# Performance work log

Hardware: AMD Instinct MI355X
Metric: run time of the kernel (lower is better)

## Reference

```python
import jax, jax.numpy as jnp
import numpy as np
from jax import lax

B, N, C_IN = 8, 16384, 32
NPOINT = 1024
RADII = (0.5, 1.0)
NSAMPLES = (16, 32)
MLPS = ((35, 32, 64), (35, 64, 128))  # first dim includes +3 for use_xyz


def setup_inputs():
    key = jax.random.key(0)
    ks = jax.random.split(key, 20)
    inp = {
        'xyz': jax.random.normal(ks[0], (B, N, 3), jnp.float32),
        'features': jax.random.normal(ks[1], (B, C_IN, N), jnp.float32),
    }
    i = 2
    for bi, spec in enumerate(MLPS):
        for li in range(len(spec) - 1):
            cin, cout = spec[li], spec[li + 1]
            inp['w%d_%d' % (bi, li)] = jax.random.normal(ks[i], (cout, cin), jnp.float32) * np.float32(1.0 / np.sqrt(cin)); i += 1
            inp['s%d_%d' % (bi, li)] = jax.random.uniform(ks[i], (cout,), jnp.float32, minval=0.5, maxval=1.5); i += 1
            inp['b%d_%d' % (bi, li)] = jax.random.normal(ks[i], (cout,), jnp.float32) * 0.1; i += 1
    return inp


def _fps(xyz, npoint):
    # iterative D-FPS, start from index 0 (matches CUDA furthest_point_sampling)
    Bb, Nn, _ = xyz.shape
    def body(carry, _):
        dists, far = carry
        centroid = jnp.take_along_axis(xyz, far[:, None, None], axis=1)  # (B,1,3)
        d = jnp.sum((xyz - centroid) ** 2, axis=-1)                       # (B,N)
        dists = jnp.minimum(dists, d)
        return (dists, jnp.argmax(dists, axis=-1).astype(jnp.int32)), far
    init = (jnp.full((Bb, Nn), 1e10, jnp.float32), jnp.zeros((Bb,), jnp.int32))
    _, idx = lax.scan(body, init, None, length=npoint)
    return idx.T  # (B, npoint)


def _ball_query(dist2, radius, nsample):
    # first-nsample-in-index-order semantics of pointnet2 ball_query;
    # empty slots padded with first hit (0 if no hit at all)
    Nn = dist2.shape[-1]
    scores = jnp.where(dist2 < radius * radius, jnp.arange(Nn, dtype=jnp.int32), Nn)
    neg, _ = lax.top_k(-scores, nsample)  # nsample smallest indices
    idx = -neg
    first = jnp.where(idx[..., :1] == Nn, 0, idx[..., :1])
    return jnp.where(idx == Nn, first, idx)


def _forward(xyz, features, params):
    fwx = jnp.concatenate([xyz.transpose(0, 2, 1), features], axis=1)   # (B,3+C,N)
    fps_idx = _fps(xyz, NPOINT)                                          # (B,P) int32
    new_xyz = jnp.take_along_axis(xyz, fps_idx[:, :, None], axis=1)      # (B,P,3)
    # pairwise squared distances via gemm (B,P,N)
    xx = jnp.sum(xyz * xyz, axis=-1)
    qq = jnp.sum(new_xyz * new_xyz, axis=-1)
    dist2 = qq[:, :, None] + xx[:, None, :] - 2.0 * jnp.einsum('bpd,bnd->bpn', new_xyz, xyz)
    centers = new_xyz.transpose(0, 2, 1)[..., None]                      # (B,3,P,1)
    outs = []
    for k in range(len(RADII)):
        idx = _ball_query(dist2, RADII[k], NSAMPLES[k])                  # (B,P,S)
        grouped = jax.vmap(lambda f, i: f[:, i])(fwx, idx)               # (B,3+C,P,S)
        x = jnp.concatenate([grouped[:, :3] - centers, grouped[:, 3:]], axis=1)
        for (w, s, b) in params[k]:
            # 1x1 Conv2d (no bias) + eval-mode BN folded into (s,b) + ReLU
            x = jax.nn.relu(jnp.einsum('oc,bcps->bops', w, x) * s[None, :, None, None] + b[None, :, None, None])
        outs.append(jnp.max(x, axis=-1))                                 # max_pool over nsample
    return new_xyz, jnp.concatenate(outs, axis=1)                        # (B,P,3), (B,192,P)


def reference(xyz, features, w0_0, s0_0, b0_0, w0_1, s0_1, b0_1, w1_0, s1_0, b1_0, w1_1, s1_1, b1_1):
    params = [[(w0_0, s0_0, b0_0), (w0_1, s0_1, b0_1)],
              [(w1_0, s1_0, b1_0), (w1_1, s1_1, b1_1)]]
    return _forward(xyz, features, params)
```

## Files before the change

### kernel.cpp

```cpp
#include <hip/hip_runtime.h>

#define B 8
#define N 16384
#define C_IN 32
#define P 1024

typedef float v2f __attribute__((ext_vector_type(2)));
typedef unsigned long long ull;

#define R8(OP) OP(0) OP(1) OP(2) OP(3) OP(4) OP(5) OP(6) OP(7)

__device__ __forceinline__ v2f pk_add(v2f a, v2f b) {
  v2f d; asm("v_pk_add_f32 %0, %1, %2" : "=v"(d) : "v"(a), "v"(b)); return d;
}
__device__ __forceinline__ v2f pk_mul(v2f a, v2f b) {
  v2f d; asm("v_pk_mul_f32 %0, %1, %2" : "=v"(d) : "v"(a), "v"(b)); return d;
}
__device__ __forceinline__ float negf(float x) {
  return __int_as_float(__float_as_int(x) ^ 0x80000000);
}

template <int CTRL>
__device__ __forceinline__ float dpp_fmax(float v) {
  float o = __int_as_float(__builtin_amdgcn_update_dpp(
      __float_as_int(v), __float_as_int(v), CTRL, 0xF, 0xF, false));
  return fmaxf(v, o);
}

__global__ __launch_bounds__(1024)
void fps_kernel(const float* __restrict__ xyz, float* __restrict__ new_xyz)
{
  __shared__ __align__(16) float sx[N];
  __shared__ __align__(16) float sy[N];
  __shared__ ull slot[2];

  const int b = blockIdx.x;
  const int t = threadIdx.x;
  const float* xb = xyz + (size_t)b * (N * 3);

  if (t == 0) { slot[0] = ~0ull; slot[1] = ~0ull; }

#define FPS_DECL(j) v2f pzp##j, dmp##j; dmp##j.x = 1e10f; dmp##j.y = 1e10f;
  R8(FPS_DECL)
#define FPS_LOADP(j) {                                                         \
    const int n0 = (t << 2) + ((j >> 1) << 12) + ((j & 1) << 1);               \
    const float2 ld0 = *(const float2*)&xb[(size_t)n0 * 3 + 0];     \
    const float2 ld1 = *(const float2*)&xb[(size_t)n0 * 3 + 2];     \
    const float2 ld2 = *(const float2*)&xb[(size_t)n0 * 3 + 4];     \
    sx[n0]     = ld0.x;  sy[n0]     = ld0.y;                                   \
    sx[n0 + 1] = ld1.y;  sy[n0 + 1] = ld2.x;                                   \
    pzp##j.x   = ld1.x;  pzp##j.y   = ld2.y;                                   \
    asm volatile("" : "+v"(pzp##j)); }
  R8(FPS_LOADP)

  float cz = xb[2];
  __syncthreads();
  float cx = sx[0], cy = sy[0];
  int sel = 0, msel = 0;

  for (int iter = 0; iter < P; ++iter) {
    msel = (t == iter) ? sel : msel;
    if (iter == P - 1) break;

    v2f cxx, cyy, czz;
    { float v = negf(cx); cxx.x = v; cxx.y = v; }
    { float v = negf(cy); cyy.x = v; cyy.y = v; }
    { float v = negf(cz); czz.x = v; czz.y = v; }

    v2f sq0, sq1, sq2, sq3, sq4, sq5, sq6, sq7;
#define FPS_XY(i, ja, jb) {                                                    \
      const int n0 = (t << 2) + ((i) << 12);                                   \
      v2f xl = *(const v2f*)&sx[n0];  v2f xh = *(const v2f*)&sx[n0 + 2];       \
      v2f yl = *(const v2f*)&sy[n0];  v2f yh = *(const v2f*)&sy[n0 + 2];       \
      v2f dxl = pk_add(xl, cxx), dyl = pk_add(yl, cyy);                        \
      v2f dxh = pk_add(xh, cxx), dyh = pk_add(yh, cyy);                        \
      sq##ja = pk_add(pk_mul(dxl, dxl), pk_mul(dyl, dyl));                     \
      sq##jb = pk_add(pk_mul(dxh, dxh), pk_mul(dyh, dyh)); }
    FPS_XY(0, 0, 1)
    FPS_XY(1, 2, 3)
    FPS_XY(2, 4, 5)
    FPS_XY(3, 6, 7)

    float bestv = -1.0f;
    int   s = 0;
#define FPS_Z(j) {                                                             \
      v2f dz = pk_add(pzp##j, czz);                                            \
      v2f dd = pk_add(sq##j, pk_mul(dz, dz));                                  \
      dmp##j.x = fminf(dmp##j.x, dd.x);                                        \
      dmp##j.y = fminf(dmp##j.y, dd.y);                                        \
      bool b0 = dmp##j.x > bestv;                                              \
      bestv = b0 ? dmp##j.x : bestv;  s = b0 ? (2 * (j))     : s;              \
      bool b1 = dmp##j.y > bestv;                                              \
      bestv = b1 ? dmp##j.y : bestv;  s = b1 ? (2 * (j) + 1) : s; }
    R8(FPS_Z)

    float wm = bestv;
    wm = dpp_fmax<0xB1>(wm);
    wm = dpp_fmax<0x4E>(wm);
    wm = dpp_fmax<0x141>(wm);
    wm = dpp_fmax<0x140>(wm);
    wm = dpp_fmax<0x142>(wm);
    wm = dpp_fmax<0x143>(wm);
    const float wmax = __int_as_float(
        __builtin_amdgcn_readlane(__float_as_int(wm), 63));

    if (bestv == wmax) {
      int nn = (t << 2) + ((s & 12) << 10) + (s & 3);
      unsigned inv = ~__float_as_uint(bestv);
      ull key = ((ull)(unsigned)(P - 1 - iter) << 46) |
                ((ull)inv << 14) | (ull)(unsigned)nn;
      atomicMin(&slot[iter & 1], key);
    }
    __syncthreads();

    ull k = slot[iter & 1];
    sel = __builtin_amdgcn_readfirstlane((int)((unsigned)k & 0x3FFFu));
    cx = sx[sel];
    cy = sy[sel];
    cz = xb[(size_t)sel * 3 + 2];
  }

  {
    const int n = msel;
    size_t o = ((size_t)b * P + t) * 3;
    new_xyz[o + 0] = sx[n];
    new_xyz[o + 1] = sy[n];
    new_xyz[o + 2] = xb[(size_t)n * 3 + 2];
  }
#undef FPS_DECL
#undef FPS_LOADP
#undef FPS_XY
#undef FPS_Z
}

__global__ __launch_bounds__(256) void ballq_kernel(
    const float* __restrict__ xyz, const float* __restrict__ new_xyz,
    int* __restrict__ idx0, int* __restrict__ idx1)
{
  const int wid  = blockIdx.x * 4 + (threadIdx.x >> 6);
  const int lane = threadIdx.x & 63;
  const int b = wid >> 10;
  const int p = wid & (P - 1);
  const float* xb = xyz + (size_t)b * (N * 3);
  const size_t bp = (size_t)b * P + p;
  const float cx = new_xyz[bp * 3 + 0];
  const float cy = new_xyz[bp * 3 + 1];
  const float cz = new_xyz[bp * 3 + 2];
  const float qv = __fadd_rn(__fadd_rn(__fmul_rn(cx, cx), __fmul_rn(cy, cy)),
                             __fmul_rn(cz, cz));
  int* __restrict__ o0 = idx0 + bp * 16;
  int* __restrict__ o1 = idx1 + bp * 32;

  int c0 = 0, c1 = 0, f0 = 0, f1 = 0;
  const unsigned long long below = (1ull << lane) - 1ull;

  for (int base = 0; base < N; base += 64) {
    int n = base + lane;
    float x = xb[n * 3 + 0], y = xb[n * 3 + 1], z = xb[n * 3 + 2];
    float xxv = __fadd_rn(__fadd_rn(__fmul_rn(x, x), __fmul_rn(y, y)),
                          __fmul_rn(z, z));
    float dot = __fadd_rn(__fadd_rn(__fmul_rn(cx, x), __fmul_rn(cy, y)),
                          __fmul_rn(cz, z));
    float d2 = __fsub_rn(__fadd_rn(qv, xxv), __fmul_rn(2.0f, dot));
    unsigned long long m0 = __ballot(d2 < 0.25f);
    unsigned long long m1 = __ballot(d2 < 1.0f);
    if (c0 == 0 && m0) f0 = base + __builtin_ctzll(m0);
    if (c1 == 0 && m1) f1 = base + __builtin_ctzll(m1);
    if ((m0 >> lane) & 1ull) {
      int pos = c0 + (int)__builtin_popcountll(m0 & below);
      if (pos < 16) o0[pos] = n;
    }
    if ((m1 >> lane) & 1ull) {
      int pos = c1 + (int)__builtin_popcountll(m1 & below);
      if (pos < 32) o1[pos] = n;
    }
    c0 = min(16, c0 + (int)__builtin_popcountll(m0));
    c1 = min(32, c1 + (int)__builtin_popcountll(m1));
    if (c0 >= 16 && c1 >= 32) break;
  }
  for (int s = c0 + lane; s < 16; s += 64) o0[s] = f0;
  for (int s = c1 + lane; s < 32; s += 64) o1[s] = f1;
}

template <int S, int C1, int C2, int CH_OFF>
__global__ __launch_bounds__(256) void mlp_kernel(
    const float* __restrict__ xyz, const float* __restrict__ feats,
    const float* __restrict__ new_xyz, const int* __restrict__ idx,
    const float* __restrict__ w1, const float* __restrict__ s1,
    const float* __restrict__ b1, const float* __restrict__ w2,
    const float* __restrict__ s2, const float* __restrict__ b2,
    float* __restrict__ out)
{
  static_assert((C1 * S) % 256 == 0 && (C2 * S) % 256 == 0, "mapping");
  __shared__ float wl1[35][C1];
  __shared__ float wl2[C1][C2];
  __shared__ float sb1[2][C1];
  __shared__ float sb2[2][C2];
  __shared__ float xs[35][S];
  __shared__ float o1s[C1][S];
  __shared__ float pm[256];

  const int tid = threadIdx.x;
  for (int i = tid; i < 35 * C1; i += 256) {
    int o = i % C1, c = i / C1;
    wl1[c][o] = w1[o * 35 + c];
  }
  for (int i = tid; i < C1 * C2; i += 256) {
    int o = i % C2, c = i / C2;
    wl2[c][o] = w2[o * C1 + c];
  }
  if (tid < C1) { sb1[0][tid] = s1[tid]; sb1[1][tid] = b1[tid]; }
  if (tid < C2) { sb2[0][tid] = s2[tid]; sb2[1][tid] = b2[tid]; }

  const int b  = blockIdx.x / (P / 8);
  const int p0 = (blockIdx.x % (P / 8)) * 8;
  const float* xb = xyz + (size_t)b * (N * 3);
  const float* fb = feats + (size_t)b * (C_IN * N);
  __syncthreads();

  for (int pi = 0; pi < 8; ++pi) {
    const int p = p0 + pi;
    const size_t bp = (size_t)b * P + p;
    const int* ip = idx + bp * S;
    const float cx = new_xyz[bp * 3 + 0];
    const float cy = new_xyz[bp * 3 + 1];
    const float cz = new_xyz[bp * 3 + 2];
    for (int i = tid; i < 35 * S; i += 256) {
      int c = i / S, s = i % S;
      int n = ip[s];
      float v;
      if (c == 0)      v = xb[n * 3 + 0] - cx;
      else if (c == 1) v = xb[n * 3 + 1] - cy;
      else if (c == 2) v = xb[n * 3 + 2] - cz;
      else             v = fb[(size_t)(c - 3) * N + n];
      xs[c][s] = v;
    }
    __syncthreads();
    {
      constexpr int OPT = (C1 * S) / 256;
      const int s  = tid % S;
      const int ob = (tid / S) * OPT;
      float acc[OPT];
#pragma unroll
      for (int j = 0; j < OPT; ++j) acc[j] = 0.0f;
      for (int c = 0; c < 35; ++c) {
        float xv = xs[c][s];
#pragma unroll
        for (int j = 0; j < OPT; ++j) acc[j] = fmaf(xv, wl1[c][ob + j], acc[j]);
      }
#pragma unroll
      for (int j = 0; j < OPT; ++j) {
        float v = fmaf(acc[j], sb1[0][ob + j], sb1[1][ob + j]);
        o1s[ob + j][s] = fmaxf(v, 0.0f);
      }
    }
    __syncthreads();
    {
      constexpr int NS = (C2 * S) / 256;
      const int o2 = tid % C2;
      const int sb = (tid / C2) * NS;
      float acc[NS];
#pragma unroll
      for (int j = 0; j < NS; ++j) acc[j] = 0.0f;
      for (int c = 0; c < C1; ++c) {
        float wv = wl2[c][o2];
#pragma unroll
        for (int j = 0; j < NS; ++j) acc[j] = fmaf(wv, o1s[c][sb + j], acc[j]);
      }
      const float scale = sb2[0][o2], bias = sb2[1][o2];
      float m = 0.0f;
#pragma unroll
      for (int j = 0; j < NS; ++j) {
        float v = fmaf(acc[j], scale, bias);
        m = fmaxf(m, v);
      }
      pm[tid] = m;
      __syncthreads();
      if (tid < C2) {
        float mm = pm[tid];
#pragma unroll
        for (int g = 1; g < 256 / C2; ++g) mm = fmaxf(mm, pm[tid + g * C2]);
        out[((size_t)b * 192 + CH_OFF + tid) * P + p] = mm;
      }
    }
    __syncthreads();
  }
}

extern "C" void kernel_launch(void* const* d_in, const int* in_sizes, int n_in,
                              void* d_out, int out_size, void* d_ws, size_t ws_size,
                              hipStream_t stream) {
  const float* xyz   = (const float*)d_in[0];
  const float* feats = (const float*)d_in[1];
  const float* w0_0 = (const float*)d_in[2];
  const float* s0_0 = (const float*)d_in[3];
  const float* b0_0 = (const float*)d_in[4];
  const float* w0_1 = (const float*)d_in[5];
  const float* s0_1 = (const float*)d_in[6];
  const float* b0_1 = (const float*)d_in[7];
  const float* w1_0 = (const float*)d_in[8];
  const float* s1_0 = (const float*)d_in[9];
  const float* b1_0 = (const float*)d_in[10];
  const float* w1_1 = (const float*)d_in[11];
  const float* s1_1 = (const float*)d_in[12];
  const float* b1_1 = (const float*)d_in[13];

  float* out      = (float*)d_out;
  float* new_xyz  = out;
  float* feat_out = out + (size_t)B * P * 3;

  char* w = (char*)d_ws;
  int* idx0 = (int*)w; w += (size_t)B * P * 16 * sizeof(int);
  int* idx1 = (int*)w; w += (size_t)B * P * 32 * sizeof(int);

  fps_kernel<<<dim3(B), dim3(1024), 0, stream>>>(xyz, new_xyz);
  ballq_kernel<<<dim3(B * P / 4), dim3(256), 0, stream>>>(xyz, new_xyz, idx0, idx1);
  mlp_kernel<16, 32, 64, 0><<<dim3(B * P / 8), dim3(256), 0, stream>>>(
      xyz, feats, new_xyz, idx0, w0_0, s0_0, b0_0, w0_1, s0_1, b0_1, feat_out);
  mlp_kernel<32, 64, 128, 64><<<dim3(B * P / 8), dim3(256), 0, stream>>>(
      xyz, feats, new_xyz, idx1, w1_0, s1_0, b1_0, w1_1, s1_1, b1_1, feat_out);
}
```

Before: 2.285 ms.

## Transpose features to point-major layout and use packed FMA in MLP kernels

Adds a transpose kernel that rewrites features from channel-major to point-major order, so the MLP gather loads each neighbour's 32 channels as contiguous float4 reads instead of 32 strided scalar loads. The MLP inner loops switch to v_pk_fma_f32 on two-wide vectors. Weight loading is vectorised and wl2 is padded by one column to reduce LDS bank conflicts. The cost is an extra kernel launch and a full pass over the feature tensor into workspace, though the total run is likely dominated by the serial FPS kernel.

```diff
diff --git a/kernel.cpp b/kernel.cpp
--- a/kernel.cpp
+++ b/kernel.cpp
@@ -131,6 +131,38 @@
 #undef FPS_LOADP
 #undef FPS_XY
 #undef FPS_Z
+}
+
+__global__ __launch_bounds__(256) void tr_kernel(
+    const float* __restrict__ feats, float* __restrict__ ftr)
+{
+  __shared__ float tile[32][65];
+  const int tid = threadIdx.x;
+  const int b  = blockIdx.x >> 8;
+  const int n0 = (blockIdx.x & 255) << 6;
+  const float* fb = feats + (size_t)b * (C_IN * N);
+
+  const int c  = tid >> 3;
+  const int nn = (tid & 7) << 3;
+  const float* src = fb + (size_t)c * N + n0 + nn;
+  const float4 a0 = *(const float4*)(src);
+  const float4 a1 = *(const float4*)(src + 4);
+  tile[c][nn + 0] = a0.x; tile[c][nn + 1] = a0.y;
+  tile[c][nn + 2] = a0.z; tile[c][nn + 3] = a0.w;
+  tile[c][nn + 4] = a1.x; tile[c][nn + 5] = a1.y;
+  tile[c][nn + 6] = a1.z; tile[c][nn + 7] = a1.w;
+  __syncthreads();
+
+  const int n  = tid >> 2;
+  const int c0 = (tid & 3) << 3;
+  float4 o0, o1;
+  o0.x = tile[c0 + 0][n]; o0.y = tile[c0 + 1][n];
+  o0.z = tile[c0 + 2][n]; o0.w = tile[c0 + 3][n];
+  o1.x = tile[c0 + 4][n]; o1.y = tile[c0 + 5][n];
+  o1.z = tile[c0 + 6][n]; o1.w = tile[c0 + 7][n];
+  float4* dst = (float4*)(ftr + ((size_t)b * N + n0 + n) * 32 + c0);
+  dst[0] = o0;
+  dst[1] = o1;
 }
 
 __global__ __launch_bounds__(256) void ballq_kernel(
@@ -184,16 +216,16 @@
 
 template <int S, int C1, int C2, int CH_OFF>
 __global__ __launch_bounds__(256) void mlp_kernel(
-    const float* __restrict__ xyz, const float* __restrict__ feats,
+    const float* __restrict__ xyz, const float* __restrict__ ftr,
     const float* __restrict__ new_xyz, const int* __restrict__ idx,
     const float* __restrict__ w1, const float* __restrict__ s1,
     const float* __restrict__ b1, const float* __restrict__ w2,
     const float* __restrict__ s2, const float* __restrict__ b2,
     float* __restrict__ out)
 {
-  static_assert((C1 * S) % 256 == 0 && (C2 * S) % 256 == 0, "mapping");
+  static_assert((C1 * S) % 512 == 0 && (C2 * S) % 512 == 0, "mapping");
   __shared__ float wl1[35][C1];
-  __shared__ float wl2[C1][C2];
+  __shared__ float wl2[C1][C2 + 1];
   __shared__ float sb1[2][C1];
   __shared__ float sb2[2][C2];
   __shared__ float xs[35][S];
@@ -205,9 +237,11 @@
     int o = i % C1, c = i / C1;
     wl1[c][o] = w1[o * 35 + c];
   }
-  for (int i = tid; i < C1 * C2; i += 256) {
-    int o = i % C2, c = i / C2;
-    wl2[c][o] = w2[o * C1 + c];
+  for (int i = tid; i < (C1 * C2) / 4; i += 256) {
+    const float4 v = *(const float4*)&w2[i * 4];
+    const int o = (i * 4) / C1, c = (i * 4) % C1;
+    wl2[c + 0][o] = v.x; wl2[c + 1][o] = v.y;
+    wl2[c + 2][o] = v.z; wl2[c + 3][o] = v.w;
   }
   if (tid < C1) { sb1[0][tid] = s1[tid]; sb1[1][tid] = b1[tid]; }
   if (tid < C2) { sb2[0][tid] = s2[tid]; sb2[1][tid] = b2[tid]; }
@@ -215,7 +249,7 @@
   const int b  = blockIdx.x / (P / 8);
   const int p0 = (blockIdx.x % (P / 8)) * 8;
   const float* xb = xyz + (size_t)b * (N * 3);
-  const float* fb = feats + (size_t)b * (C_IN * N);
+  const float* fb = ftr + (size_t)b * N * 32;
   __syncthreads();
 
   for (int pi = 0; pi < 8; ++pi) {
@@ -225,56 +259,75 @@
     const float cx = new_xyz[bp * 3 + 0];
     const float cy = new_xyz[bp * 3 + 1];
     const float cz = new_xyz[bp * 3 + 2];
-    for (int i = tid; i < 35 * S; i += 256) {
-      int c = i / S, s = i % S;
-      int n = ip[s];
-      float v;
-      if (c == 0)      v = xb[n * 3 + 0] - cx;
-      else if (c == 1) v = xb[n * 3 + 1] - cy;
-      else if (c == 2) v = xb[n * 3 + 2] - cz;
-      else             v = fb[(size_t)(c - 3) * N + n];
-      xs[c][s] = v;
+    for (int s2 = tid; s2 < S; s2 += 256) {
+      const int n = ip[s2];
+      xs[0][s2] = xb[n * 3 + 0] - cx;
+      xs[1][s2] = xb[n * 3 + 1] - cy;
+      xs[2][s2] = xb[n * 3 + 2] - cz;
+    }
+    for (int i = tid; i < S * 8; i += 256) {
+      const int s = i >> 3, q = i & 7;
+      const int n = ip[s];
+      const float4 v = *(const float4*)&fb[(size_t)n * 32 + q * 4];
+      const int c = 3 + q * 4;
+      xs[c + 0][s] = v.x; xs[c + 1][s] = v.y;
+      xs[c + 2][s] = v.z; xs[c + 3][s] = v.w;
     }
     __syncthreads();
     {
-      constexpr int OPT = (C1 * S) / 256;
+      constexpr int OPT  = (C1 * S) / 256;
+      constexpr int OPT2 = OPT / 2;
       const int s  = tid % S;
       const int ob = (tid / S) * OPT;
-      float acc[OPT];
-#pragma unroll
-      for (int j = 0; j < OPT; ++j) acc[j] = 0.0f;
+      v2f acc[OPT2];
+#pragma unroll
+      for (int m = 0; m < OPT2; ++m) { acc[m].x = 0.0f; acc[m].y = 0.0f; }
       for (int c = 0; c < 35; ++c) {
-        float xv = xs[c][s];
-#pragma unroll
-        for (int j = 0; j < OPT; ++j) acc[j] = fmaf(xv, wl1[c][ob + j], acc[j]);
-      }
-#pragma unroll
-      for (int j = 0; j < OPT; ++j) {
-        float v = fmaf(acc[j], sb1[0][ob + j], sb1[1][ob + j]);
-        o1s[ob + j][s] = fmaxf(v, 0.0f);
+        const float xv = xs[c][s];
+        v2f xv2; xv2.x = xv; xv2.y = xv;
+#pragma unroll
+        for (int m = 0; m < OPT2; ++m) {
+          const v2f w = *(const v2f*)&wl1[c][ob + 2 * m];
+          asm("v_pk_fma_f32 %0, %1, %2, %0"
+              : "+v"(acc[m]) : "v"(xv2), "v"(w));
+        }
+      }
+#pragma unroll
+      for (int m = 0; m < OPT2; ++m) {
+        const int o0i = ob + 2 * m, o1i = ob + 2 * m + 1;
+        float v0 = fmaf(acc[m].x, sb1[0][o0i], sb1[1][o0i]);
+        float v1 = fmaf(acc[m].y, sb1[0][o1i], sb1[1][o1i]);
+        o1s[o0i][s] = fmaxf(v0, 0.0f);
+        o1s[o1i][s] = fmaxf(v1, 0.0f);
       }
     }
     __syncthreads();
     {
-      constexpr int NS = (C2 * S) / 256;
+      constexpr int NS  = (C2 * S) / 256;
+      constexpr int NS2 = NS / 2;
       const int o2 = tid % C2;
       const int sb = (tid / C2) * NS;
-      float acc[NS];
-#pragma unroll
-      for (int j = 0; j < NS; ++j) acc[j] = 0.0f;
+      v2f acc[NS2];
+#pragma unroll
+      for (int m = 0; m < NS2; ++m) { acc[m].x = 0.0f; acc[m].y = 0.0f; }
       for (int c = 0; c < C1; ++c) {
-        float wv = wl2[c][o2];
-#pragma unroll
-        for (int j = 0; j < NS; ++j) acc[j] = fmaf(wv, o1s[c][sb + j], acc[j]);
+        const float wv = wl2[c][o2];
+        v2f wv2; wv2.x = wv; wv2.y = wv;
+#pragma unroll
+        for (int m = 0; m < NS2; ++m) {
+          const v2f ov = *(const v2f*)&o1s[c][sb + 2 * m];
+          asm("v_pk_fma_f32 %0, %1, %2, %0"
+              : "+v"(acc[m]) : "v"(wv2), "v"(ov));
+        }
       }
       const float scale = sb2[0][o2], bias = sb2[1][o2];
-      float m = 0.0f;
-#pragma unroll
-      for (int j = 0; j < NS; ++j) {
-        float v = fmaf(acc[j], scale, bias);
-        m = fmaxf(m, v);
-      }
-      pm[tid] = m;
+      float m2 = 0.0f;
+#pragma unroll
+      for (int m = 0; m < NS2; ++m) {
+        m2 = fmaxf(m2, fmaf(acc[m].x, scale, bias));
+        m2 = fmaxf(m2, fmaf(acc[m].y, scale, bias));
+      }
+      pm[tid] = m2;
       __syncthreads();
       if (tid < C2) {
         float mm = pm[tid];
@@ -310,13 +363,15 @@
   float* feat_out = out + (size_t)B * P * 3;
 
   char* w = (char*)d_ws;
+  float* ftr = (float*)w; w += (size_t)B * N * 32 * sizeof(float);
   int* idx0 = (int*)w; w += (size_t)B * P * 16 * sizeof(int);
   int* idx1 = (int*)w; w += (size_t)B * P * 32 * sizeof(int);
 
+  tr_kernel<<<dim3(B * (N / 64)), dim3(256), 0, stream>>>(feats, ftr);
   fps_kernel<<<dim3(B), dim3(1024), 0, stream>>>(xyz, new_xyz);
   ballq_kernel<<<dim3(B * P / 4), dim3(256), 0, stream>>>(xyz, new_xyz, idx0, idx1);
   mlp_kernel<16, 32, 64, 0><<<dim3(B * P / 8), dim3(256), 0, stream>>>(
-      xyz, feats, new_xyz, idx0, w0_0, s0_0, b0_0, w0_1, s0_1, b0_1, feat_out);
+      xyz, ftr, new_xyz, idx0, w0_0, s0_0, b0_0, w0_1, s0_1, b0_1, feat_out);
   mlp_kernel<32, 64, 128, 64><<<dim3(B * P / 8), dim3(256), 0, stream>>>(
-      xyz, feats, new_xyz, idx1, w1_0, s1_0, b1_0, w1_1, s1_1, b1_1, feat_out);
-}
+      xyz, ftr, new_xyz, idx1, w1_0, s1_0, b1_0, w1_1, s1_1, b1_1, feat_out);
+}
```

New measurement: 2.308 ms. About the same (+1.0%).
